# Optimization experiments

Hardware: AMD Instinct MI355X
Metric: run time of the kernel (lower is better)

The kernel has to match this reference:

```python
import jax, jax.numpy as jnp
import numpy as np

N0, N1, N2, N3 = 100000, 25000, 6250, 1600
DEG = 16
D_IN, D_H = 512, 256


def setup_inputs() -> dict:
    key = jax.random.key(0)
    ks = jax.random.split(key, 20)
    inp = {}
    inp["x"] = jax.random.normal(ks[0], (N0, D_IN), dtype=jnp.float32)
    # bipartite blocks: (src_ids into previous frontier, dst_ids into next frontier)
    inp["src0"] = jax.random.randint(ks[1], (N1 * DEG,), 0, N0)
    inp["dst0"] = jax.random.randint(ks[2], (N1 * DEG,), 0, N1)
    inp["src1"] = jax.random.randint(ks[3], (N2 * DEG,), 0, N1)
    inp["dst1"] = jax.random.randint(ks[4], (N2 * DEG,), 0, N2)
    inp["src2"] = jax.random.randint(ks[5], (N3 * DEG,), 0, N2)
    inp["dst2"] = jax.random.randint(ks[6], (N3 * DEG,), 0, N3)
    def xavier(k, shp):
        fan_in, fan_out = shp
        lim = jnp.sqrt(6.0 / (fan_in + fan_out))
        return jax.random.uniform(k, shp, jnp.float32, -lim, lim)
    inp["Ws0"] = xavier(ks[7], (D_IN, D_H)); inp["Wn0"] = xavier(ks[8], (D_IN, D_H)); inp["b0"] = jnp.zeros((D_H,), jnp.float32)
    inp["Ws1"] = xavier(ks[9], (D_H, D_H)); inp["Wn1"] = xavier(ks[10], (D_H, D_H)); inp["b1"] = jnp.zeros((D_H,), jnp.float32)
    inp["Ws2"] = xavier(ks[11], (D_H, D_H)); inp["Wn2"] = xavier(ks[12], (D_H, D_H)); inp["b2"] = jnp.zeros((D_H,), jnp.float32)
    inp["W_fc"] = xavier(ks[13], (D_H, D_H)); inp["b_fc"] = jnp.zeros((D_H,), jnp.float32)
    return inp


def _sage_mean(h, src, dst, n_dst, Ws, Wn, b):
    # DGL SAGEConv('mean') on a bipartite block: out = h_dst@Ws + mean_neigh@Wn + b
    h_dst = h[:n_dst]                                   # [n_dst, d]
    msg = h[src]                                        # [E, d] gather
    agg = jax.ops.segment_sum(msg, dst, num_segments=n_dst)
    deg = jax.ops.segment_sum(jnp.ones(src.shape, h.dtype), dst, num_segments=n_dst)
    mean = agg / jnp.maximum(deg, 1.0)[:, None]
    return h_dst @ Ws + mean @ Wn + b


def reference(x, src0, dst0, src1, dst1, src2, dst2,
              Ws0, Wn0, b0, Ws1, Wn1, b1, Ws2, Wn2, b2, W_fc, b_fc):
    h = _sage_mean(x, src0, dst0, N1, Ws0, Wn0, b0)
    h = jax.nn.relu(h)  # dropout is identity in eval mode
    h = _sage_mean(h, src1, dst1, N2, Ws1, Wn1, b1)
    h = jax.nn.relu(h)
    h = _sage_mean(h, src2, dst2, N3, Ws2, Wn2, b2)
    return h @ W_fc + b_fc
```

## Files before the change

kernel.cpp:

```cpp
#include <hip/hip_runtime.h>
#include <hip/hip_bf16.h>
#include <cstddef>
#include <cstdint>

#define N0 100000
#define N1 25000
#define N2 6250
#define N3 1600
#define DEG 16
#define D_IN 512
#define D_H 256

#define E0 (N1*DEG)
#define E1 (N2*DEG)
#define E2 (N3*DEG)

typedef _Float16 half_t;
typedef __attribute__((ext_vector_type(8))) _Float16 f16x8;
typedef __attribute__((ext_vector_type(4))) float f32x4;

#define XB 25000
#define WB 2304
#define HB (((E0+E1+E2) + 255) / 256)

__global__ __launch_bounds__(256)
void mega_conv_kernel(const float* __restrict__ x, half_t* __restrict__ xh,
                      const float* s0, const float* s1, const float* s2, const float* s3,
                      const float* s4, const float* s5, const float* s6,
                      half_t* t0, half_t* t1, half_t* t2, half_t* t3,
                      half_t* t4, half_t* t5, half_t* t6,
                      const int* __restrict__ d0, const int* __restrict__ d1,
                      const int* __restrict__ d2,
                      int* __restrict__ c0, int* __restrict__ c1, int* __restrict__ c2)
{
    const int bid = blockIdx.x;
    if (bid < XB) {
        const int id = bid * 256 + threadIdx.x;
        const float4* p = reinterpret_cast<const float4*>(x) + (size_t)id * 2;
        const float4 a = p[0], b = p[1];
        f16x8 o;
        o[0] = (half_t)a.x; o[1] = (half_t)a.y; o[2] = (half_t)a.z; o[3] = (half_t)a.w;
        o[4] = (half_t)b.x; o[5] = (half_t)b.y; o[6] = (half_t)b.z; o[7] = (half_t)b.w;
        *(reinterpret_cast<f16x8*>(xh) + id) = o;
    } else if (bid < XB + WB) {
        const int id = (bid - XB) * 256 + threadIdx.x;
        const float* src; half_t* dst; int kb; int e;
        if (id < 131072)      { src = s0; dst = t0; kb = 9; e = id; }
        else if (id < 262144) { src = s1; dst = t1; kb = 9; e = id - 131072; }
        else if (id < 327680) { src = s2; dst = t2; kb = 8; e = id - 262144; }
        else if (id < 393216) { src = s3; dst = t3; kb = 8; e = id - 327680; }
        else if (id < 458752) { src = s4; dst = t4; kb = 8; e = id - 393216; }
        else if (id < 524288) { src = s5; dst = t5; kb = 8; e = id - 458752; }
        else if (id < 589824) { src = s6; dst = t6; kb = 8; e = id - 524288; }
        else return;
        const int K = 1 << kb;
        const int nn = e >> kb, k = e & (K - 1);
        dst[((size_t)nn << kb) + k] = (half_t)src[(size_t)k * 256 + nn];
    } else {
        const int i = (bid - XB - WB) * 256 + threadIdx.x;
        if (i < E0)                atomicAdd(&c0[d0[i]], 1);
        else if (i < E0 + E1)      atomicAdd(&c1[d1[i - E0]], 1);
        else if (i < E0 + E1 + E2) atomicAdd(&c2[d2[i - E0 - E1]], 1);
    }
}

__global__ void fill3_kernel(const int* __restrict__ s0, const int* __restrict__ d0,
                             const int* __restrict__ s1, const int* __restrict__ d1,
                             const int* __restrict__ s2, const int* __restrict__ d2,
                             int* __restrict__ u0, int* __restrict__ u1, int* __restrict__ u2,
                             int* __restrict__ e0, int* __restrict__ e1, int* __restrict__ e2)
{
    const int i = blockIdx.x * 256 + threadIdx.x;
    if (i < E0) {
        const int p = atomicAdd(&u0[d0[i]], 1); e0[p] = s0[i];
    } else if (i < E0 + E1) {
        const int j = i - E0;
        const int p = atomicAdd(&u1[d1[j]], 1); e1[p] = s1[j];
    } else if (i < E0 + E1 + E2) {
        const int j = i - E0 - E1;
        const int p = atomicAdd(&u2[d2[j]], 1); e2[p] = s2[j];
    }
}

__global__ __launch_bounds__(1024)
void scan3_kernel(const int* __restrict__ c0, int* __restrict__ p0, int* __restrict__ u0,
                  const int* __restrict__ c1, int* __restrict__ p1, int* __restrict__ u1,
                  const int* __restrict__ c2, int* __restrict__ p2, int* __restrict__ u2)
{
    const int b = blockIdx.x;
    const int* cnt = (b == 0) ? c0 : (b == 1) ? c1 : c2;
    int* ptr = (b == 0) ? p0 : (b == 1) ? p1 : p2;
    int* cur = (b == 0) ? u0 : (b == 1) ? u1 : u2;
    const int n = (b == 0) ? N1 : (b == 1) ? N2 : N3;

    const int t = threadIdx.x;
    const int chunk = (n + 1023) >> 10;
    const int beg = t * chunk;
    const int end = min(n, beg + chunk);

    int sum = 0;
    for (int i = beg; i < end; ++i) sum += cnt[i];

    const int lane = t & 63, wid = t >> 6;
    int inc = sum;
    #pragma unroll
    for (int d = 1; d < 64; d <<= 1) {
        int u = __shfl_up(inc, d, 64);
        if (lane >= d) inc += u;
    }
    __shared__ int wtot[16];
    __shared__ int total_s;
    if (lane == 63) wtot[wid] = inc;
    __syncthreads();
    if (wid == 0) {
        int w = (lane < 16) ? wtot[lane] : 0;
        int ws = w;
        #pragma unroll
        for (int d = 1; d < 16; d <<= 1) {
            int u = __shfl_up(ws, d, 64);
            if (lane >= d) ws += u;
        }
        if (lane < 16) wtot[lane] = ws - w;
        if (lane == 15) total_s = ws;
    }
    __syncthreads();
    int run = (inc - sum) + wtot[wid];
    for (int i = beg; i < end; ++i) {
        ptr[i] = run; cur[i] = run;
        run += cnt[i];
    }
    if (t == 0) ptr[n] = total_s;
}

template<int K>
__global__ __launch_bounds__(256)
void csr_mean_f16(const half_t* __restrict__ h, const int* __restrict__ esrc,
                  const int* __restrict__ ptr, half_t* __restrict__ mean, int n)
{
    constexpr int TPN = K / 8;
    constexpr int NPB = 256 / TPN;
    const int node = blockIdx.x * NPB + threadIdx.x / TPN;
    const int lane = threadIdx.x % TPN;
    if (node >= n) return;
    const int beg = ptr[node], end = ptr[node + 1];
    float acc[8] = {};
    for (int base = beg; base < end; base += TPN) {
        const int rem = end - base;
        const int cnt = (rem < TPN) ? rem : TPN;
        const int myidx = (lane < cnt) ? esrc[base + lane] : 0;
        int j = 0;
        for (; j + 3 < cnt; j += 4) {
            const int a0 = __shfl(myidx, j + 0, TPN);
            const int a1 = __shfl(myidx, j + 1, TPN);
            const int a2 = __shfl(myidx, j + 2, TPN);
            const int a3 = __shfl(myidx, j + 3, TPN);
            const f16x8 v0 = *reinterpret_cast<const f16x8*>(h + (size_t)a0 * K + (size_t)lane * 8);
            const f16x8 v1 = *reinterpret_cast<const f16x8*>(h + (size_t)a1 * K + (size_t)lane * 8);
            const f16x8 v2 = *reinterpret_cast<const f16x8*>(h + (size_t)a2 * K + (size_t)lane * 8);
            const f16x8 v3 = *reinterpret_cast<const f16x8*>(h + (size_t)a3 * K + (size_t)lane * 8);
            #pragma unroll
            for (int i = 0; i < 8; ++i) acc[i] += (float)v0[i];
            #pragma unroll
            for (int i = 0; i < 8; ++i) acc[i] += (float)v1[i];
            #pragma unroll
            for (int i = 0; i < 8; ++i) acc[i] += (float)v2[i];
            #pragma unroll
            for (int i = 0; i < 8; ++i) acc[i] += (float)v3[i];
        }
        for (; j < cnt; ++j) {
            const int a0 = __shfl(myidx, j, TPN);
            const f16x8 v0 = *reinterpret_cast<const f16x8*>(h + (size_t)a0 * K + (size_t)lane * 8);
            #pragma unroll
            for (int i = 0; i < 8; ++i) acc[i] += (float)v0[i];
        }
    }
    const float r = 1.0f / fmaxf((float)(end - beg), 1.0f);
    f16x8 o;
    #pragma unroll
    for (int i = 0; i < 8; ++i) o[i] = (half_t)(acc[i] * r);
    *reinterpret_cast<f16x8*>(mean + (size_t)node * K + (size_t)lane * 8) = o;
}

#define GBM 64
#define GBK 32
#define LPAD 40

template<bool HAS_MEAN, bool RELU, bool OUT_F16>
__global__ __launch_bounds__(512)
void mfma_gemm(const half_t* __restrict__ A,
               const half_t* __restrict__ Mn,
               const half_t* __restrict__ WsT,
               const half_t* __restrict__ WnT,
               const float* __restrict__ bias,
               void* __restrict__ Cout,
               int M, int K)
{
    __shared__ half_t sA[GBM][LPAD];
    __shared__ half_t sB[256][LPAD];

    const int tid  = threadIdx.x;
    const int wid  = tid >> 6;
    const int lane = tid & 63;
    const int bm   = blockIdx.x * GBM;

    f32x4 acc[4][2] = {};

    const int npass = HAS_MEAN ? 2 : 1;
    for (int pass = 0; pass < npass; ++pass) {
        const half_t* __restrict__ Ap = pass ? Mn : A;
        const half_t* __restrict__ Wp = pass ? WnT : WsT;

        for (int k0 = 0; k0 < K; k0 += GBK) {
            if (tid < 256) {
                const int row = tid >> 2;
                const int kq  = (tid & 3) * 8;
                f16x8 v = {};
                if (bm + row < M)
                    v = *reinterpret_cast<const f16x8*>(Ap + (size_t)(bm + row) * K + k0 + kq);
                *reinterpret_cast<f16x8*>(&sA[row][kq]) = v;
            }
            {
                const int kq = (tid & 3) * 8;
                const int r0 = tid >> 2;
                #pragma unroll
                for (int j = 0; j < 2; ++j) {
                    const int row = r0 + 128 * j;
                    const f16x8 v = *reinterpret_cast<const f16x8*>(Wp + (size_t)row * K + k0 + kq);
                    *reinterpret_cast<f16x8*>(&sB[row][kq]) = v;
                }
            }
            __syncthreads();

            const int lrow = lane & 15;
            const int koff = (lane >> 4) * 8;
            f16x8 af[4], bf[2];
            #pragma unroll
            for (int m = 0; m < 4; ++m)
                af[m] = *reinterpret_cast<const f16x8*>(&sA[m * 16 + lrow][koff]);
            #pragma unroll
            for (int n = 0; n < 2; ++n)
                bf[n] = *reinterpret_cast<const f16x8*>(&sB[wid * 32 + n * 16 + lrow][koff]);
            #pragma unroll
            for (int m = 0; m < 4; ++m)
                #pragma unroll
                for (int n = 0; n < 2; ++n)
                    acc[m][n] = __builtin_amdgcn_mfma_f32_16x16x32_f16(af[m], bf[n], acc[m][n], 0, 0, 0);
            __syncthreads();
        }
    }

    const int lcol = lane & 15;
    const int rgrp = lane >> 4;
    #pragma unroll
    for (int m = 0; m < 4; ++m) {
        #pragma unroll
        for (int n = 0; n < 2; ++n) {
            const int col = wid * 32 + n * 16 + lcol;
            const float bv = bias[col];
            #pragma unroll
            for (int r = 0; r < 4; ++r) {
                const int row = bm + m * 16 + rgrp * 4 + r;
                if (row >= M) continue;
                float v = acc[m][n][r] + bv;
                if (RELU) v = fmaxf(v, 0.0f);
                if (OUT_F16) ((half_t*)Cout)[(size_t)row * 256 + col] = (half_t)v;
                else         ((float*)Cout)[(size_t)row * 256 + col] = v;
            }
        }
    }
}

static constexpr size_t align256(size_t x) { return (x + 255) & ~(size_t)255; }

extern "C" void kernel_launch(void* const* d_in, const int* in_sizes, int n_in,
                              void* d_out, int out_size, void* d_ws, size_t ws_size,
                              hipStream_t stream)
{
    const float* x    = (const float*)d_in[0];
    const int*  src0  = (const int*)d_in[1];
    const int*  dst0  = (const int*)d_in[2];
    const int*  src1  = (const int*)d_in[3];
    const int*  dst1  = (const int*)d_in[4];
    const int*  src2  = (const int*)d_in[5];
    const int*  dst2  = (const int*)d_in[6];
    const float* Ws0  = (const float*)d_in[7];
    const float* Wn0  = (const float*)d_in[8];
    const float* b0   = (const float*)d_in[9];
    const float* Ws1  = (const float*)d_in[10];
    const float* Wn1  = (const float*)d_in[11];
    const float* b1   = (const float*)d_in[12];
    const float* Ws2  = (const float*)d_in[13];
    const float* Wn2  = (const float*)d_in[14];
    const float* b2   = (const float*)d_in[15];
    const float* W_fc = (const float*)d_in[16];
    const float* b_fc = (const float*)d_in[17];
    float* out = (float*)d_out;

    char* ws = (char*)d_ws;
    size_t off = 0;
    const size_t cntA_off = off; off = align256(off + (size_t)(N1 + N2 + N3) * 4);
    const size_t ptr0_off = off; off = align256(off + (size_t)(N1 + 1) * 4);
    const size_t ptr1_off = off; off = align256(off + (size_t)(N2 + 1) * 4);
    const size_t ptr2_off = off; off = align256(off + (size_t)(N3 + 1) * 4);
    const size_t cur0_off = off; off = align256(off + (size_t)N1 * 4);
    const size_t cur1_off = off; off = align256(off + (size_t)N2 * 4);
    const size_t cur2_off = off; off = align256(off + (size_t)N3 * 4);
    const size_t es0_off  = off; off = align256(off + (size_t)E0 * 4);
    const size_t es1_off  = off; off = align256(off + (size_t)E1 * 4);
    const size_t es2_off  = off; off = align256(off + (size_t)E2 * 4);
    const size_t xh_off   = off; off = align256(off + (size_t)N0 * D_IN * 2);
    const size_t mean_off = off; off = align256(off + (size_t)N1 * D_IN * 2);
    const size_t h0_off   = off; off = align256(off + (size_t)N1 * D_H * 2);
    const size_t h1_off   = off; off = align256(off + (size_t)N2 * D_H * 2);
    const size_t h2_off   = off; off = align256(off + (size_t)N3 * D_H * 2);
    const size_t wt0_off  = off; off = align256(off + (size_t)D_IN * D_H * 2);
    const size_t wt1_off  = off; off = align256(off + (size_t)D_IN * D_H * 2);
    const size_t wt2_off  = off; off = align256(off + (size_t)D_H * D_H * 2);
    const size_t wt3_off  = off; off = align256(off + (size_t)D_H * D_H * 2);
    const size_t wt4_off  = off; off = align256(off + (size_t)D_H * D_H * 2);
    const size_t wt5_off  = off; off = align256(off + (size_t)D_H * D_H * 2);
    const size_t wt6_off  = off; off = align256(off + (size_t)D_H * D_H * 2);

    int* cnt0 = (int*)(ws + cntA_off);
    int* cnt1 = cnt0 + N1;
    int* cnt2 = cnt1 + N2;
    int* ptr0 = (int*)(ws + ptr0_off);
    int* ptr1 = (int*)(ws + ptr1_off);
    int* ptr2 = (int*)(ws + ptr2_off);
    int* cur0 = (int*)(ws + cur0_off);
    int* cur1 = (int*)(ws + cur1_off);
    int* cur2 = (int*)(ws + cur2_off);
    int* es0  = (int*)(ws + es0_off);
    int* es1  = (int*)(ws + es1_off);
    int* es2  = (int*)(ws + es2_off);
    half_t* xh   = (half_t*)(ws + xh_off);
    half_t* mean = (half_t*)(ws + mean_off);
    half_t* h0   = (half_t*)(ws + h0_off);
    half_t* h1   = (half_t*)(ws + h1_off);
    half_t* h2   = (half_t*)(ws + h2_off);
    half_t* WsT0 = (half_t*)(ws + wt0_off);
    half_t* WnT0 = (half_t*)(ws + wt1_off);
    half_t* WsT1 = (half_t*)(ws + wt2_off);
    half_t* WnT1 = (half_t*)(ws + wt3_off);
    half_t* WsT2 = (half_t*)(ws + wt4_off);
    half_t* WnT2 = (half_t*)(ws + wt5_off);
    half_t* WfcT = (half_t*)(ws + wt6_off);

    hipMemsetAsync(cnt0, 0, (size_t)(N1 + N2 + N3) * 4, stream);
    mega_conv_kernel<<<XB + WB + HB, 256, 0, stream>>>(
        x, xh,
        Ws0, Wn0, Ws1, Wn1, Ws2, Wn2, W_fc,
        WsT0, WnT0, WsT1, WnT1, WsT2, WnT2, WfcT,
        dst0, dst1, dst2, cnt0, cnt1, cnt2);
    scan3_kernel<<<3, 1024, 0, stream>>>(cnt0, ptr0, cur0, cnt1, ptr1, cur1, cnt2, ptr2, cur2);
    {
        const int tot = E0 + E1 + E2;
        fill3_kernel<<<(tot + 255) / 256, 256, 0, stream>>>(
            src0, dst0, src1, dst1, src2, dst2, cur0, cur1, cur2, es0, es1, es2);
    }

    {
        constexpr int NPB = 256 / (D_IN / 8);
        csr_mean_f16<D_IN><<<(N1 + NPB - 1) / NPB, 256, 0, stream>>>(xh, es0, ptr0, mean, N1);
        mfma_gemm<true, true, true><<<(N1 + GBM - 1) / GBM, 512, 0, stream>>>(
            xh, mean, WsT0, WnT0, b0, h0, N1, D_IN);
    }
    {
        constexpr int NPB = 256 / (D_H / 8);
        csr_mean_f16<D_H><<<(N2 + NPB - 1) / NPB, 256, 0, stream>>>(h0, es1, ptr1, mean, N2);
        mfma_gemm<true, true, true><<<(N2 + GBM - 1) / GBM, 512, 0, stream>>>(
            h0, mean, WsT1, WnT1, b1, h1, N2, D_H);
    }
    {
        constexpr int NPB = 256 / (D_H / 8);
        csr_mean_f16<D_H><<<(N3 + NPB - 1) / NPB, 256, 0, stream>>>(h1, es2, ptr2, mean, N3);
        mfma_gemm<true, false, true><<<(N3 + GBM - 1) / GBM, 512, 0, stream>>>(
            h1, mean, WsT2, WnT2, b2, h2, N3, D_H);
    }
    mfma_gemm<false, false, false><<<(N3 + GBM - 1) / GBM, 512, 0, stream>>>(
        h2, nullptr, WfcT, nullptr, b_fc, out, N3, D_H);
}
```

Measured before the change: 309.1 us.

## Enlarge GEMM tiles, load direct-to-LDS with XOR swizzle, unroll gather by eight

The MFMA GEMM now uses 128x64 block tiles with a 4x2 wave layout, where each wave computes a 32x128 sub-tile. Operands are staged with global_load_lds 16-byte async copies into an XOR-swizzled LDS layout instead of padded register-staged stores. This is meant to raise data reuse per LDS load and cut the number of load instructions and bank conflicts. The CSR mean-gather kernel also unrolls to eight outstanding row loads per lane to expose more memory-level parallelism. The A-tile load drops its row bounds check, so the last partial block reads past M rows. Those values are discarded, but the reads could go out of bounds.

```diff
diff --git a/kernel.cpp b/kernel.cpp
--- a/kernel.cpp
+++ b/kernel.cpp
@@ -22,6 +22,14 @@
 #define XB 25000
 #define WB 2304
 #define HB (((E0+E1+E2) + 255) / 256)
+
+__device__ __forceinline__ void gl_lds16(const void* g, void* l)
+{
+    __builtin_amdgcn_global_load_lds(
+        (const __attribute__((address_space(1))) void*)g,
+        (__attribute__((address_space(3))) void*)l,
+        16, 0, 0);
+}
 
 __global__ __launch_bounds__(256)
 void mega_conv_kernel(const float* __restrict__ x, half_t* __restrict__ xh,
@@ -149,23 +157,18 @@
         const int cnt = (rem < TPN) ? rem : TPN;
         const int myidx = (lane < cnt) ? esrc[base + lane] : 0;
         int j = 0;
-        for (; j + 3 < cnt; j += 4) {
-            const int a0 = __shfl(myidx, j + 0, TPN);
-            const int a1 = __shfl(myidx, j + 1, TPN);
-            const int a2 = __shfl(myidx, j + 2, TPN);
-            const int a3 = __shfl(myidx, j + 3, TPN);
-            const f16x8 v0 = *reinterpret_cast<const f16x8*>(h + (size_t)a0 * K + (size_t)lane * 8);
-            const f16x8 v1 = *reinterpret_cast<const f16x8*>(h + (size_t)a1 * K + (size_t)lane * 8);
-            const f16x8 v2 = *reinterpret_cast<const f16x8*>(h + (size_t)a2 * K + (size_t)lane * 8);
-            const f16x8 v3 = *reinterpret_cast<const f16x8*>(h + (size_t)a3 * K + (size_t)lane * 8);
-            #pragma unroll
-            for (int i = 0; i < 8; ++i) acc[i] += (float)v0[i];
-            #pragma unroll
-            for (int i = 0; i < 8; ++i) acc[i] += (float)v1[i];
-            #pragma unroll
-            for (int i = 0; i < 8; ++i) acc[i] += (float)v2[i];
-            #pragma unroll
-            for (int i = 0; i < 8; ++i) acc[i] += (float)v3[i];
+        for (; j + 7 < cnt; j += 8) {
+            int a[8];
+            #pragma unroll
+            for (int u = 0; u < 8; ++u) a[u] = __shfl(myidx, j + u, TPN);
+            f16x8 v[8];
+            #pragma unroll
+            for (int u = 0; u < 8; ++u)
+                v[u] = *reinterpret_cast<const f16x8*>(h + (size_t)a[u] * K + (size_t)lane * 8);
+            #pragma unroll
+            for (int u = 0; u < 8; ++u)
+                #pragma unroll
+                for (int i = 0; i < 8; ++i) acc[i] += (float)v[u][i];
         }
         for (; j < cnt; ++j) {
             const int a0 = __shfl(myidx, j, TPN);
@@ -181,9 +184,8 @@
     *reinterpret_cast<f16x8*>(mean + (size_t)node * K + (size_t)lane * 8) = o;
 }
 
-#define GBM 64
-#define GBK 32
-#define LPAD 40
+#define GBM 128
+#define GBK 64
 
 template<bool HAS_MEAN, bool RELU, bool OUT_F16>
 __global__ __launch_bounds__(512)
@@ -195,15 +197,20 @@
                void* __restrict__ Cout,
                int M, int K)
 {
-    __shared__ half_t sA[GBM][LPAD];
-    __shared__ half_t sB[256][LPAD];
+    __shared__ half_t sA[GBM * GBK];
+    __shared__ half_t sB[256 * GBK];
 
     const int tid  = threadIdx.x;
     const int wid  = tid >> 6;
     const int lane = tid & 63;
+    const int wm   = wid >> 1;
+    const int wn   = wid & 1;
     const int bm   = blockIdx.x * GBM;
 
-    f32x4 acc[4][2] = {};
+    const int lrow = lane & 15;
+    const int kg16 = (lane >> 4) << 4;
+
+    f32x4 acc[2][8] = {};
 
     const int npass = HAS_MEAN ? 2 : 1;
     for (int pass = 0; pass < npass; ++pass) {
@@ -211,55 +218,57 @@
         const half_t* __restrict__ Wp = pass ? WnT : WsT;
 
         for (int k0 = 0; k0 < K; k0 += GBK) {
-            if (tid < 256) {
-                const int row = tid >> 2;
-                const int kq  = (tid & 3) * 8;
-                f16x8 v = {};
-                if (bm + row < M)
-                    v = *reinterpret_cast<const f16x8*>(Ap + (size_t)(bm + row) * K + k0 + kq);
-                *reinterpret_cast<f16x8*>(&sA[row][kq]) = v;
+            #pragma unroll
+            for (int i = 0; i < 2; ++i) {
+                const int Lb = ((i << 3) + wid) << 10;
+                const int L  = Lb + (lane << 4);
+                const int row = L >> 7;
+                const int c   = (L & 127) ^ ((row & 7) << 4);
+                gl_lds16(Ap + (size_t)(bm + row) * K + k0 + (c >> 1), sA + (Lb >> 1));
             }
-            {
-                const int kq = (tid & 3) * 8;
-                const int r0 = tid >> 2;
+            #pragma unroll
+            for (int i = 0; i < 4; ++i) {
+                const int Lb = ((i << 3) + wid) << 10;
+                const int L  = Lb + (lane << 4);
+                const int row = L >> 7;
+                const int c   = (L & 127) ^ ((row & 7) << 4);
+                gl_lds16(Wp + (size_t)row * K + k0 + (c >> 1), sB + (Lb >> 1));
+            }
+            __syncthreads();
+
+            #pragma unroll
+            for (int kk = 0; kk < 2; ++kk) {
+                const int cb = (kk << 6) + kg16;
+                f16x8 af[2];
                 #pragma unroll
-                for (int j = 0; j < 2; ++j) {
-                    const int row = r0 + 128 * j;
-                    const f16x8 v = *reinterpret_cast<const f16x8*>(Wp + (size_t)row * K + k0 + kq);
-                    *reinterpret_cast<f16x8*>(&sB[row][kq]) = v;
+                for (int m = 0; m < 2; ++m) {
+                    const int row = wm * 32 + m * 16 + lrow;
+                    const int c = cb ^ ((row & 7) << 4);
+                    af[m] = *reinterpret_cast<const f16x8*>(&sA[row * GBK + (c >> 1)]);
+                }
+                #pragma unroll
+                for (int n = 0; n < 8; ++n) {
+                    const int row = wn * 128 + n * 16 + lrow;
+                    const int c = cb ^ ((row & 7) << 4);
+                    const f16x8 bf = *reinterpret_cast<const f16x8*>(&sB[row * GBK + (c >> 1)]);
+                    acc[0][n] = __builtin_amdgcn_mfma_f32_16x16x32_f16(af[0], bf, acc[0][n], 0, 0, 0);
+                    acc[1][n] = __builtin_amdgcn_mfma_f32_16x16x32_f16(af[1], bf, acc[1][n], 0, 0, 0);
                 }
             }
             __syncthreads();
-
-            const int lrow = lane & 15;
-            const int koff = (lane >> 4) * 8;
-            f16x8 af[4], bf[2];
-            #pragma unroll
-            for (int m = 0; m < 4; ++m)
-                af[m] = *reinterpret_cast<const f16x8*>(&sA[m * 16 + lrow][koff]);
-            #pragma unroll
-            for (int n = 0; n < 2; ++n)
-                bf[n] = *reinterpret_cast<const f16x8*>(&sB[wid * 32 + n * 16 + lrow][koff]);
-            #pragma unroll
-            for (int m = 0; m < 4; ++m)
-                #pragma unroll
-                for (int n = 0; n < 2; ++n)
-                    acc[m][n] = __builtin_amdgcn_mfma_f32_16x16x32_f16(af[m], bf[n], acc[m][n], 0, 0, 0);
-            __syncthreads();
-        }
-    }
-
-    const int lcol = lane & 15;
+        }
+    }
+
     const int rgrp = lane >> 4;
     #pragma unroll
-    for (int m = 0; m < 4; ++m) {
+    for (int n = 0; n < 8; ++n) {
+        const int col = wn * 128 + n * 16 + lrow;
+        const float bv = bias[col];
         #pragma unroll
-        for (int n = 0; n < 2; ++n) {
-            const int col = wid * 32 + n * 16 + lcol;
-            const float bv = bias[col];
+        for (int m = 0; m < 2; ++m) {
             #pragma unroll
             for (int r = 0; r < 4; ++r) {
-                const int row = bm + m * 16 + rgrp * 4 + r;
+                const int row = bm + wm * 32 + m * 16 + rgrp * 4 + r;
                 if (row >= M) continue;
                 float v = acc[m][n][r] + bv;
                 if (RELU) v = fmaxf(v, 0.0f);
```

New measurement: 319.8 us. 1.03x slower.

## Overlap neighbor gather with self-GEMM in one launch, add partial in second GEMM

Applied to the files above, without the earlier changes.

Layers 0 and 1 now run a combined kernel. Some blocks compute the neighbor mean gather while the remaining blocks compute h_dst@Ws+b into an fp32 partial buffer. A second GEMM then computes mean@Wn, adds the partial and applies ReLU, so the memory-bound gather overlaps with MFMA work. The gather loop is also unrolled to 8 outstanding loads per step. The cost is an extra fp32 partial write and read, plus a mixed block role that may unbalance scheduling.

```diff
diff --git a/kernel.cpp b/kernel.cpp
--- a/kernel.cpp
+++ b/kernel.cpp
@@ -132,44 +132,36 @@
     if (t == 0) ptr[n] = total_s;
 }
 
-template<int K>
-__global__ __launch_bounds__(256)
-void csr_mean_f16(const half_t* __restrict__ h, const int* __restrict__ esrc,
-                  const int* __restrict__ ptr, half_t* __restrict__ mean, int n)
-{
-    constexpr int TPN = K / 8;
-    constexpr int NPB = 256 / TPN;
-    const int node = blockIdx.x * NPB + threadIdx.x / TPN;
-    const int lane = threadIdx.x % TPN;
+template<int K, int TPN>
+__device__ __forceinline__ void gather_mean_node(
+    const half_t* __restrict__ feat, const int* __restrict__ esrc,
+    const int* __restrict__ ptr, half_t* __restrict__ mean,
+    int node, int gl, int n)
+{
     if (node >= n) return;
     const int beg = ptr[node], end = ptr[node + 1];
     float acc[8] = {};
     for (int base = beg; base < end; base += TPN) {
         const int rem = end - base;
         const int cnt = (rem < TPN) ? rem : TPN;
-        const int myidx = (lane < cnt) ? esrc[base + lane] : 0;
+        const int myidx = (gl < cnt) ? esrc[base + gl] : 0;
         int j = 0;
-        for (; j + 3 < cnt; j += 4) {
-            const int a0 = __shfl(myidx, j + 0, TPN);
-            const int a1 = __shfl(myidx, j + 1, TPN);
-            const int a2 = __shfl(myidx, j + 2, TPN);
-            const int a3 = __shfl(myidx, j + 3, TPN);
-            const f16x8 v0 = *reinterpret_cast<const f16x8*>(h + (size_t)a0 * K + (size_t)lane * 8);
-            const f16x8 v1 = *reinterpret_cast<const f16x8*>(h + (size_t)a1 * K + (size_t)lane * 8);
-            const f16x8 v2 = *reinterpret_cast<const f16x8*>(h + (size_t)a2 * K + (size_t)lane * 8);
-            const f16x8 v3 = *reinterpret_cast<const f16x8*>(h + (size_t)a3 * K + (size_t)lane * 8);
-            #pragma unroll
-            for (int i = 0; i < 8; ++i) acc[i] += (float)v0[i];
-            #pragma unroll
-            for (int i = 0; i < 8; ++i) acc[i] += (float)v1[i];
-            #pragma unroll
-            for (int i = 0; i < 8; ++i) acc[i] += (float)v2[i];
-            #pragma unroll
-            for (int i = 0; i < 8; ++i) acc[i] += (float)v3[i];
+        for (; j + 7 < cnt; j += 8) {
+            int a[8];
+            #pragma unroll
+            for (int u = 0; u < 8; ++u) a[u] = __shfl(myidx, j + u, TPN);
+            f16x8 v[8];
+            #pragma unroll
+            for (int u = 0; u < 8; ++u)
+                v[u] = *reinterpret_cast<const f16x8*>(feat + (size_t)a[u] * K + (size_t)gl * 8);
+            #pragma unroll
+            for (int u = 0; u < 8; ++u)
+                #pragma unroll
+                for (int i = 0; i < 8; ++i) acc[i] += (float)v[u][i];
         }
         for (; j < cnt; ++j) {
             const int a0 = __shfl(myidx, j, TPN);
-            const f16x8 v0 = *reinterpret_cast<const f16x8*>(h + (size_t)a0 * K + (size_t)lane * 8);
+            const f16x8 v0 = *reinterpret_cast<const f16x8*>(feat + (size_t)a0 * K + (size_t)gl * 8);
             #pragma unroll
             for (int i = 0; i < 8; ++i) acc[i] += (float)v0[i];
         }
@@ -178,20 +170,33 @@
     f16x8 o;
     #pragma unroll
     for (int i = 0; i < 8; ++i) o[i] = (half_t)(acc[i] * r);
-    *reinterpret_cast<f16x8*>(mean + (size_t)node * K + (size_t)lane * 8) = o;
+    *reinterpret_cast<f16x8*>(mean + (size_t)node * K + (size_t)gl * 8) = o;
+}
+
+template<int K>
+__global__ __launch_bounds__(256)
+void csr_mean_f16(const half_t* __restrict__ h, const int* __restrict__ esrc,
+                  const int* __restrict__ ptr, half_t* __restrict__ mean, int n)
+{
+    constexpr int TPN = K / 8;
+    constexpr int NPB = 256 / TPN;
+    gather_mean_node<K, TPN>(h, esrc, ptr, mean,
+                             blockIdx.x * NPB + threadIdx.x / TPN,
+                             threadIdx.x % TPN, n);
 }
 
 #define GBM 64
 #define GBK 32
 #define LPAD 40
 
-template<bool HAS_MEAN, bool RELU, bool OUT_F16>
+template<bool HAS_MEAN, bool RELU, bool OUT_F16, bool ADDP>
 __global__ __launch_bounds__(512)
 void mfma_gemm(const half_t* __restrict__ A,
                const half_t* __restrict__ Mn,
                const half_t* __restrict__ WsT,
                const half_t* __restrict__ WnT,
                const float* __restrict__ bias,
+               const float* __restrict__ Pin,
                void* __restrict__ Cout,
                int M, int K)
 {
@@ -207,8 +212,8 @@
 
     const int npass = HAS_MEAN ? 2 : 1;
     for (int pass = 0; pass < npass; ++pass) {
-        const half_t* __restrict__ Ap = pass ? Mn : A;
-        const half_t* __restrict__ Wp = pass ? WnT : WsT;
+        const half_t* __restrict__ Ap = (HAS_MEAN && pass) ? Mn : A;
+        const half_t* __restrict__ Wp = (HAS_MEAN && pass) ? WnT : WsT;
 
         for (int k0 = 0; k0 < K; k0 += GBK) {
             if (tid < 256) {
@@ -256,15 +261,97 @@
         #pragma unroll
         for (int n = 0; n < 2; ++n) {
             const int col = wid * 32 + n * 16 + lcol;
-            const float bv = bias[col];
+            const float bv = ADDP ? 0.0f : bias[col];
             #pragma unroll
             for (int r = 0; r < 4; ++r) {
                 const int row = bm + m * 16 + rgrp * 4 + r;
                 if (row >= M) continue;
-                float v = acc[m][n][r] + bv;
+                float v = acc[m][n][r] + (ADDP ? Pin[(size_t)row * 256 + col] : bv);
                 if (RELU) v = fmaxf(v, 0.0f);
                 if (OUT_F16) ((half_t*)Cout)[(size_t)row * 256 + col] = (half_t)v;
                 else         ((float*)Cout)[(size_t)row * 256 + col] = v;
+            }
+        }
+    }
+}
+
+template<int K>
+__global__ __launch_bounds__(512)
+void gather_gemm(const half_t* __restrict__ feat,
+                 const int* __restrict__ esrc, const int* __restrict__ ptr,
+                 half_t* __restrict__ mean, int n_dst,
+                 const half_t* __restrict__ WsT, const float* __restrict__ bias,
+                 float* __restrict__ P, int GB)
+{
+    __shared__ half_t sA[GBM][LPAD];
+    __shared__ half_t sB[256][LPAD];
+
+    const int tid = threadIdx.x;
+    if (blockIdx.x < GB) {
+        constexpr int TPN = K / 8;
+        constexpr int NPB = 512 / TPN;
+        gather_mean_node<K, TPN>(feat, esrc, ptr, mean,
+                                 blockIdx.x * NPB + tid / TPN, tid % TPN, n_dst);
+        return;
+    }
+
+    const int wid  = tid >> 6;
+    const int lane = tid & 63;
+    const int bm   = (blockIdx.x - GB) * GBM;
+
+    f32x4 acc[4][2] = {};
+
+    for (int k0 = 0; k0 < K; k0 += GBK) {
+        if (tid < 256) {
+            const int row = tid >> 2;
+            const int kq  = (tid & 3) * 8;
+            f16x8 v = {};
+            if (bm + row < n_dst)
+                v = *reinterpret_cast<const f16x8*>(feat + (size_t)(bm + row) * K + k0 + kq);
+            *reinterpret_cast<f16x8*>(&sA[row][kq]) = v;
+        }
+        {
+            const int kq = (tid & 3) * 8;
+            const int r0 = tid >> 2;
+            #pragma unroll
+            for (int j = 0; j < 2; ++j) {
+                const int row = r0 + 128 * j;
+                const f16x8 v = *reinterpret_cast<const f16x8*>(WsT + (size_t)row * K + k0 + kq);
+                *reinterpret_cast<f16x8*>(&sB[row][kq]) = v;
+            }
+        }
+        __syncthreads();
+
+        const int lrow = lane & 15;
+        const int koff = (lane >> 4) * 8;
+        f16x8 af[4], bf[2];
+        #pragma unroll
+        for (int m = 0; m < 4; ++m)
+            af[m] = *reinterpret_cast<const f16x8*>(&sA[m * 16 + lrow][koff]);
+        #pragma unroll
+        for (int n = 0; n < 2; ++n)
+            bf[n] = *reinterpret_cast<const f16x8*>(&sB[wid * 32 + n * 16 + lrow][koff]);
+        #pragma unroll
+        for (int m = 0; m < 4; ++m)
+            #pragma unroll
+            for (int n = 0; n < 2; ++n)
+                acc[m][n] = __builtin_amdgcn_mfma_f32_16x16x32_f16(af[m], bf[n], acc[m][n], 0, 0, 0);
+        __syncthreads();
+    }
+
+    const int lcol = lane & 15;
+    const int rgrp = lane >> 4;
+    #pragma unroll
+    for (int m = 0; m < 4; ++m) {
+        #pragma unroll
+        for (int n = 0; n < 2; ++n) {
+            const int col = wid * 32 + n * 16 + lcol;
+            const float bv = bias[col];
+            #pragma unroll
+            for (int r = 0; r < 4; ++r) {
+                const int row = bm + m * 16 + rgrp * 4 + r;
+                if (row >= n_dst) continue;
+                P[(size_t)row * 256 + col] = acc[m][n][r] + bv;
             }
         }
     }
@@ -310,6 +397,7 @@
     const size_t es2_off  = off; off = align256(off + (size_t)E2 * 4);
     const size_t xh_off   = off; off = align256(off + (size_t)N0 * D_IN * 2);
     const size_t mean_off = off; off = align256(off + (size_t)N1 * D_IN * 2);
+    const size_t P_off    = off; off = align256(off + (size_t)N1 * D_H * 4);
     const size_t h0_off   = off; off = align256(off + (size_t)N1 * D_H * 2);
     const size_t h1_off   = off; off = align256(off + (size_t)N2 * D_H * 2);
     const size_t h2_off   = off; off = align256(off + (size_t)N3 * D_H * 2);
@@ -335,6 +423,7 @@
     int* es2  = (int*)(ws + es2_off);
     half_t* xh   = (half_t*)(ws + xh_off);
     half_t* mean = (half_t*)(ws + mean_off);
+    float*  P    = (float*)(ws + P_off);
     half_t* h0   = (half_t*)(ws + h0_off);
     half_t* h1   = (half_t*)(ws + h1_off);
     half_t* h2   = (half_t*)(ws + h2_off);
@@ -360,23 +449,28 @@
     }
 
     {
-        constexpr int NPB = 256 / (D_IN / 8);
-        csr_mean_f16<D_IN><<<(N1 + NPB - 1) / NPB, 256, 0, stream>>>(xh, es0, ptr0, mean, N1);
-        mfma_gemm<true, true, true><<<(N1 + GBM - 1) / GBM, 512, 0, stream>>>(
-            xh, mean, WsT0, WnT0, b0, h0, N1, D_IN);
+        const int GB = N1 / (512 / (D_IN / 8));
+        const int SB = (N1 + GBM - 1) / GBM;
+        gather_gemm<D_IN><<<GB + SB, 512, 0, stream>>>(
+            xh, es0, ptr0, mean, N1, WsT0, b0, P, GB);
+        mfma_gemm<false, true, true, true><<<SB, 512, 0, stream>>>(
+            mean, nullptr, WnT0, nullptr, nullptr, P, h0, N1, D_IN);
     }
     {
-        constexpr int NPB = 256 / (D_H / 8);
-        csr_mean_f16<D_H><<<(N2 + NPB - 1) / NPB, 256, 0, stream>>>(h0, es1, ptr1, mean, N2);
-        mfma_gemm<true, true, true><<<(N2 + GBM - 1) / GBM, 512, 0, stream>>>(
-            h0, mean, WsT1, WnT1, b1, h1, N2, D_H);
+        const int NPB = 512 / (D_H / 8);
+        const int GB = (N2 + NPB - 1) / NPB;
+        const int SB = (N2 + GBM - 1) / GBM;
+        gather_gemm<D_H><<<GB + SB, 512, 0, stream>>>(
+            h0, es1, ptr1, mean, N2, WsT1, b1, P, GB);
+        mfma_gemm<false, true, true, true><<<SB, 512, 0, stream>>>(
+            mean, nullptr, WnT1, nullptr, nullptr, P, h1, N2, D_H);
     }
     {
         constexpr int NPB = 256 / (D_H / 8);
         csr_mean_f16<D_H><<<(N3 + NPB - 1) / NPB, 256, 0, stream>>>(h1, es2, ptr2, mean, N3);
-        mfma_gemm<true, false, true><<<(N3 + GBM - 1) / GBM, 512, 0, stream>>>(
-            h1, mean, WsT2, WnT2, b2, h2, N3, D_H);
-    }
-    mfma_gemm<false, false, false><<<(N3 + GBM - 1) / GBM, 512, 0, stream>>>(
-        h2, nullptr, WfcT, nullptr, b_fc, out, N3, D_H);
-}
+        mfma_gemm<true, false, true, false><<<(N3 + GBM - 1) / GBM, 512, 0, stream>>>(
+            h1, mean, WsT2, WnT2, b2, nullptr, h2, N3, D_H);
+    }
+    mfma_gemm<false, false, false, false><<<(N3 + GBM - 1) / GBM, 512, 0, stream>>>(
+        h2, nullptr, WfcT, nullptr, b_fc, nullptr, out, N3, D_H);
+}
```

Result: slower. 322.4 us (+4.3%).
